# Kernel optimization log

Hardware: AMD Instinct MI355X
Metric: run time of the kernel (lower is better)

## Reference

```python
import jax, jax.numpy as jnp
import numpy as np

H = 256      # term/query/document hidden size (hardcoded .view(-1, 256) in source)
POS_DIM = 4  # nn.Embedding(15, 4)
V = 50000


def gru_cell(x, h, Wih, Whh, bih, bhh):
    """PyTorch-convention GRU cell. x: [B, Din], h: [B, H]."""
    gi = x @ Wih.T + bih
    gh = h @ Whh.T + bhh
    ir, iz, i_n = jnp.split(gi, 3, axis=-1)
    hr, hz, h_n = jnp.split(gh, 3, axis=-1)
    r = jax.nn.sigmoid(ir + hr)
    z = jax.nn.sigmoid(iz + hz)
    n = jnp.tanh(i_n + r * h_n)
    return (1.0 - z) * n + z * h


def _gru_params(key, in_dim, hid):
    k1, k2, k3, k4 = jax.random.split(key, 4)
    s = 1.0 / np.sqrt(hid)
    u = lambda k, shp: jax.random.uniform(k, shp, jnp.float32, -s, s)
    return u(k1, (3 * hid, in_dim)), u(k2, (3 * hid, hid)), u(k3, (3 * hid,)), u(k4, (3 * hid,))


def setup_inputs() -> dict:
    key = jax.random.key(0)
    ks = jax.random.split(key, 16)
    Q, Lq, P, N, Ld = 64, 20, 12, 12, 50
    inp = {}
    inp["query_tokens"] = jax.random.randint(ks[0], (Q, Lq), 0, V, dtype=jnp.int32)
    inp["pos_tokens"] = jax.random.randint(ks[1], (P, Ld), 0, V, dtype=jnp.int32)
    inp["neg_tokens"] = jax.random.randint(ks[2], (N, Ld), 0, V, dtype=jnp.int32)
    # TermEncoder: embedding + GRU cell
    inp["term_emb"] = jax.random.normal(ks[3], (V, H), jnp.float32) * 0.1
    inp["term_Wih"], inp["term_Whh"], inp["term_bih"], inp["term_bhh"] = _gru_params(ks[4], H, H)
    # ContextEncoder: embedding + two GRU cells (content c, attention a)
    inp["doc_emb"] = jax.random.normal(ks[5], (V, H), jnp.float32) * 0.1
    inp["doc_c_Wih"], inp["doc_c_Whh"], inp["doc_c_bih"], inp["doc_c_bhh"] = _gru_params(ks[6], H, H)
    inp["doc_a_Wih"], inp["doc_a_Whh"], inp["doc_a_bih"], inp["doc_a_bhh"] = _gru_params(ks[7], H, H)
    # position embedding (15, 4) + position_dense Linear(H+4 -> H)
    inp["pos_table"] = jax.random.normal(ks[8], (15, POS_DIM), jnp.float32) * 0.1
    sd = 1.0 / np.sqrt(H + POS_DIM)
    inp["posd_W"] = jax.random.uniform(ks[9], (H, H + POS_DIM), jnp.float32, -sd, sd)
    inp["posd_b"] = jax.random.uniform(ks[10], (H,), jnp.float32, -sd, sd)
    # QueryEncoder GRU cell (single step on the memory-augmented query state)
    inp["qry_Wih"], inp["qry_Whh"], inp["qry_bih"], inp["qry_bhh"] = _gru_params(ks[11], H, H)
    return inp


def reference(query_tokens, pos_tokens, neg_tokens,
              term_emb, term_Wih, term_Whh, term_bih, term_bhh,
              doc_emb, doc_c_Wih, doc_c_Whh, doc_c_bih, doc_c_bhh,
              doc_a_Wih, doc_a_Whh, doc_a_bih, doc_a_bhh,
              pos_table, posd_W, posd_b,
              qry_Wih, qry_Whh, qry_bih, qry_bhh):
    f32 = term_emb.dtype

    # --- TermEncoder: run GRU over each query's tokens (batched over Q queries) ---
    q_xs = term_emb[query_tokens]                       # [Q, Lq, H]
    h0q = jnp.zeros((query_tokens.shape[0], H), f32)
    def term_step(h, x):
        return gru_cell(x, h, term_Wih, term_Whh, term_bih, term_bhh), None
    enc_hidden, _ = jax.lax.scan(term_step, h0q, jnp.swapaxes(q_xs, 0, 1))  # [Q, H]

    # --- ContextEncoder: two parallel GRUs over each doc's tokens (batched over docs) ---
    def encode_docs(tokens):
        xs = doc_emb[tokens]                            # [D, Ld, H]
        h0 = jnp.zeros((tokens.shape[0], H), f32)
        def step(carry, x):
            hc, ha = carry
            hc = gru_cell(x, hc, doc_c_Wih, doc_c_Whh, doc_c_bih, doc_c_bhh)
            ha = gru_cell(x, ha, doc_a_Wih, doc_a_Whh, doc_a_bih, doc_a_bhh)
            return (hc, ha), None
        (hc, ha), _ = jax.lax.scan(step, (h0, h0), jnp.swapaxes(xs, 0, 1))
        # position encoding (pos_enc == 1): concat per-doc-index embedding, dense back to H
        pe = pos_table[jnp.arange(tokens.shape[0])]      # [D, 4]
        hc = jnp.concatenate([hc, pe], axis=-1) @ posd_W.T + posd_b
        return hc, ha                                    # [D, H], [D, H]

    pos_c, pos_a = encode_docs(pos_tokens)
    neg_c, neg_a = encode_docs(neg_tokens)

    # --- memory read: softmax(dot(a_vecs, q)) weighted sum of c_vecs, per query ---
    def attend(c, a_vecs, q):
        scores = q @ a_vecs.T                            # [Q, D]
        w = jax.nn.softmax(scores, axis=-1)
        return w @ c                                     # [Q, H]

    q_pos_neg = enc_hidden + attend(pos_c, pos_a, enc_hidden) + attend(neg_c, neg_a, enc_hidden)

    # --- QueryEncoder: one GRU step on the memory-augmented state ---
    h0 = jnp.zeros_like(q_pos_neg)
    q_out = gru_cell(q_pos_neg, h0, qry_Wih, qry_Whh, qry_bih, qry_bhh)  # [Q, H]
    return q_out
```

## Files before the change

kernel.cpp:

```cpp
#include <hip/hip_runtime.h>
#include <hip/hip_fp16.h>
#include <math.h>

#define H 256

typedef _Float16 h2_t __attribute__((ext_vector_type(2)));
union U16x8 { uint4 u; h2_t h[4]; };

#define WS_WTQ   0u
#define WS_PT    196608u
#define WS_WTPT  263168u
#define WS_WTPC  361472u
#define WS_WTPA  459776u
#define WS_GI_T  558080u
#define WS_GI_C  1541120u
#define WS_GI_A  2462720u
#define WS_ENC   3384320u
#define WS_HC    3400704u
#define WS_HA    3406848u
#define WS_HCP   3412992u

__device__ __forceinline__ float sigmoidf_(float x){ return 1.f/(1.f+expf(-x)); }

__global__ __launch_bounds__(256) void k_prep(
    const float* __restrict__ tWhh, const float* __restrict__ cWhh, const float* __restrict__ aWhh,
    const float* __restrict__ qWih, const float* __restrict__ pdW,
    __half* __restrict__ WTPt, __half* __restrict__ WTPc, __half* __restrict__ WTPa,
    float* __restrict__ WTq, float* __restrict__ PT)
{
    const int b = blockIdx.x, tid = threadIdx.x;
    if (b < 2304) {
        const float* in; __half* out; int j;
        if (b < 768)       { in = tWhh; out = WTPt; j = b; }
        else if (b < 1536) { in = cWhh; out = WTPc; j = b - 768; }
        else               { in = aWhh; out = WTPa; j = b - 1536; }
        float v = in[(size_t)j * 256 + tid];
        out[(size_t)(tid >> 3) * 6144 + j * 8 + (tid & 7)] = (__half)v;
        return;
    }
    __shared__ float t[64][65];
    const float* in; float* out; int R, C, bx, by;
    if (b < 2352) { int bb = b - 2304; in = qWih; out = WTq; R = 768; C = 256; bx = bb & 3; by = bb >> 2; }
    else          { int bb = b - 2352; in = pdW;  out = PT;  R = 256; C = 260; bx = bb % 5; by = bb / 5; }
    const int c0 = bx * 64, r0 = by * 64;
    const int cc = tid & 63;
    const int rr = tid >> 6;
#pragma unroll
    for (int s = 0; s < 16; s++) {
        int row = s * 4 + rr;
        if (r0 + row < R && c0 + cc < C)
            t[row][cc] = in[(size_t)(r0 + row) * C + (c0 + cc)];
    }
    __syncthreads();
#pragma unroll
    for (int s = 0; s < 16; s++) {
        int col = s * 4 + rr;
        if (c0 + col < C && r0 + cc < R)
            out[(size_t)(c0 + col) * R + (r0 + cc)] = t[cc][col];
    }
}

__global__ __launch_bounds__(256) void k_gi_gemm(
    const int* __restrict__ qtok, const int* __restrict__ ptok, const int* __restrict__ ntok,
    const float* __restrict__ temb, const float* __restrict__ demb,
    const float* __restrict__ tWih, const float* __restrict__ cWih, const float* __restrict__ aWih,
    const float* __restrict__ tbih, const float* __restrict__ cbih, const float* __restrict__ abih,
    float* __restrict__ gi_term, float* __restrict__ gi_c, float* __restrict__ gi_a)
{
    __shared__ __align__(16) float As[64][68];
    __shared__ __align__(16) float Bs[64][68];
    __shared__ int tok[64];
    __shared__ int vld[64];

    const int bid = blockIdx.x, tid = threadIdx.x;
    const float *Wih, *bih, *emb; float* out; int nrows, seg, mt, nt;
    if (bid < 240)      { seg = 0; int b = bid;       mt = b / 12; nt = b % 12; Wih = tWih; bih = tbih; emb = temb; out = gi_term; nrows = 1280; }
    else if (bid < 468) { seg = 1; int b = bid - 240; mt = b / 12; nt = b % 12; Wih = cWih; bih = cbih; emb = demb; out = gi_c;    nrows = 1200; }
    else                { seg = 2; int b = bid - 468; mt = b / 12; nt = b % 12; Wih = aWih; bih = abih; emb = demb; out = gi_a;    nrows = 1200; }

    if (tid < 64) {
        int rg = mt * 64 + tid;
        int v = rg < nrows;
        int token = 0;
        if (v) {
            if (seg == 0) { int t = rg >> 6, q = rg & 63; token = qtok[q * 20 + t]; }
            else          { int t = rg / 24, d = rg % 24; token = (d < 12) ? ptok[d * 50 + t] : ntok[(d - 12) * 50 + t]; }
        }
        tok[tid] = token; vld[tid] = v;
    }
    __syncthreads();

    float acc[4][4];
#pragma unroll
    for (int i = 0; i < 4; i++)
#pragma unroll
        for (int jj = 0; jj < 4; jj++) acc[i][jj] = 0.f;

    const int r0 = (tid >> 4) << 2;
    const int j0 = (tid & 15) << 2;
    const int jb = nt * 64;
    const int lr = tid & 15;
    const int lk = (tid >> 4) << 2;

    for (int k0 = 0; k0 < 256; k0 += 64) {
#pragma unroll
        for (int s = 0; s < 4; s++) {
            int r = lr + s * 16;
            float4 v4 = *(const float4*)(emb + (size_t)tok[r] * H + k0 + lk);
            As[lk + 0][r] = v4.x; As[lk + 1][r] = v4.y; As[lk + 2][r] = v4.z; As[lk + 3][r] = v4.w;
            float4 w4 = *(const float4*)(Wih + (size_t)(jb + r) * H + k0 + lk);
            Bs[lk + 0][r] = w4.x; Bs[lk + 1][r] = w4.y; Bs[lk + 2][r] = w4.z; Bs[lk + 3][r] = w4.w;
        }
        __syncthreads();
#pragma unroll 8
        for (int k = 0; k < 64; k++) {
            float4 av = *(const float4*)&As[k][r0];
            float4 bv = *(const float4*)&Bs[k][j0];
            acc[0][0] += av.x * bv.x; acc[0][1] += av.x * bv.y; acc[0][2] += av.x * bv.z; acc[0][3] += av.x * bv.w;
            acc[1][0] += av.y * bv.x; acc[1][1] += av.y * bv.y; acc[1][2] += av.y * bv.z; acc[1][3] += av.y * bv.w;
            acc[2][0] += av.z * bv.x; acc[2][1] += av.z * bv.y; acc[2][2] += av.z * bv.z; acc[2][3] += av.z * bv.w;
            acc[3][0] += av.w * bv.x; acc[3][1] += av.w * bv.y; acc[3][2] += av.w * bv.z; acc[3][3] += av.w * bv.w;
        }
        __syncthreads();
    }

    float4 bias = *(const float4*)(bih + jb + j0);
#pragma unroll
    for (int i = 0; i < 4; i++) {
        int r = r0 + i;
        if (!vld[r]) continue;
        int rg = mt * 64 + r;
        float4 o;
        o.x = acc[i][0] + bias.x; o.y = acc[i][1] + bias.y;
        o.z = acc[i][2] + bias.z; o.w = acc[i][3] + bias.w;
        *(float4*)(out + (size_t)rg * 768 + jb + j0) = o;
    }
}

__global__ __launch_bounds__(768, 3) void k_recur4(
    const __half* __restrict__ WTPt, const __half* __restrict__ WTPc, const __half* __restrict__ WTPa,
    const float* __restrict__ tbhh, const float* __restrict__ cbhh, const float* __restrict__ abhh,
    const float* __restrict__ gi_t, const float* __restrict__ gi_c, const float* __restrict__ gi_a,
    float* __restrict__ enc, float* __restrict__ hc, float* __restrict__ ha)
{
    __shared__ __align__(16) __half hhl[H];
    __shared__ __align__(16) float  gh[768];
    const int b = blockIdx.x, tid = threadIdx.x;
    const __half* WTP; const float *bhh, *gi; float* outp; int T, nch, chain;
    if (b < 64)      { WTP = WTPt; bhh = tbhh; gi = gi_t; T = 20; nch = 64; chain = b;      outp = enc; }
    else if (b < 88) { WTP = WTPc; bhh = cbhh; gi = gi_c; T = 50; nch = 24; chain = b - 64; outp = hc; }
    else             { WTP = WTPa; bhh = abhh; gi = gi_a; T = 50; nch = 24; chain = b - 88; outp = ha; }

    const float bj = bhh[tid];

    const uint4* __restrict__ W4 = (const uint4*)WTP;
    uint4 w[32];
#pragma unroll
    for (int k8 = 0; k8 < 32; k8++) w[k8] = W4[k8 * 768 + tid];

    float h = 0.f;
    if (tid < H) hhl[tid] = (__half)0.f;
    __syncthreads();

    const uint4* hh4 = (const uint4*)hhl;
    const float* __restrict__ grow0 = gi + (size_t)chain * 768;
    const size_t gstride = (size_t)nch * 768;

    for (int t = 0; t < T; t++) {
        float a0 = 0.f, a1 = 0.f, a2 = 0.f, a3 = 0.f;
#pragma unroll
        for (int k8 = 0; k8 < 32; k8++) {
            U16x8 hv; hv.u = hh4[k8];
            U16x8 wv; wv.u = w[k8];
            a0 = __builtin_amdgcn_fdot2(wv.h[0], hv.h[0], a0, false);
            a1 = __builtin_amdgcn_fdot2(wv.h[1], hv.h[1], a1, false);
            a2 = __builtin_amdgcn_fdot2(wv.h[2], hv.h[2], a2, false);
            a3 = __builtin_amdgcn_fdot2(wv.h[3], hv.h[3], a3, false);
        }
        gh[tid] = bj + ((a0 + a1) + (a2 + a3));
        __syncthreads();

        if (tid < H) {
            const float* grow = grow0 + (size_t)t * gstride;
            float r = sigmoidf_(grow[tid]       + gh[tid]);
            float z = sigmoidf_(grow[tid + 256] + gh[tid + 256]);
            float n = tanhf(grow[tid + 512] + r * gh[tid + 512]);
            h = (1.f - z) * n + z * h;
            hhl[tid] = (__half)h;
        }
        __syncthreads();
    }
    if (tid < H) outp[(size_t)chain * H + tid] = h;
}

__global__ __launch_bounds__(256) void k_posd(
    const float* __restrict__ PT, const float* __restrict__ pdb,
    const float* __restrict__ ptab, const float* __restrict__ hc_raw,
    float* __restrict__ hcp)
{
    __shared__ __align__(16) float hl[260];
    const int d = blockIdx.x, j = threadIdx.x;
    if (j < 256) hl[j] = hc_raw[d * H + j];
    if (j < 4)   hl[256 + j] = ptab[(d % 12) * 4 + j];
    __syncthreads();
    float acc = pdb[j];
#pragma unroll 4
    for (int k = 0; k < 260; k++) acc += PT[(size_t)k * 256 + j] * hl[k];
    hcp[d * H + j] = acc;
}

__global__ __launch_bounds__(256) void k_final(
    const float* __restrict__ enc, const float* __restrict__ ha, const float* __restrict__ hcp,
    const float* __restrict__ WT_q, const float* __restrict__ qbih, const float* __restrict__ qbhh,
    float* __restrict__ out)
{
    __shared__ __align__(16) float ql[H];
    __shared__ float wts[24];
    __shared__ __align__(16) float qs_l[H];
    const int q = blockIdx.x, j = threadIdx.x;
    ql[j] = enc[q * H + j];
    __syncthreads();
    if (j < 192) {
        int dd = j >> 3, l8 = j & 7;
        float s = 0.f;
        for (int k = l8 * 32; k < l8 * 32 + 32; k++) s += ha[dd * H + k] * ql[k];
        s += __shfl_xor(s, 1); s += __shfl_xor(s, 2); s += __shfl_xor(s, 4);
        if (l8 == 0) wts[dd] = s;
    }
    __syncthreads();
    if (j < 2) {
        int base = j * 12;
        float m = wts[base];
        for (int d = 1; d < 12; d++) m = fmaxf(m, wts[base + d]);
        float sum = 0.f;
        for (int d = 0; d < 12; d++) { float e = expf(wts[base + d] - m); wts[base + d] = e; sum += e; }
        float inv = 1.f / sum;
        for (int d = 0; d < 12; d++) wts[base + d] *= inv;
    }
    __syncthreads();
    float qs = ql[j];
#pragma unroll 4
    for (int d = 0; d < 24; d++) qs += wts[d] * hcp[d * H + j];
    qs_l[j] = qs;
    __syncthreads();
    float ar = qbih[j], az = qbih[j + 256], an = qbih[j + 512];
    const float* wp = WT_q + j;
#pragma unroll 4
    for (int k = 0; k < H; k++) {
        float hv = qs_l[k];
        const float* wk = wp + (size_t)k * 768;
        ar += wk[0] * hv; az += wk[256] * hv; an += wk[512] * hv;
    }
    float r = sigmoidf_(ar + qbhh[j]);
    float z = sigmoidf_(az + qbhh[j + 256]);
    float n = tanhf(an + r * qbhh[j + 512]);
    out[q * H + j] = (1.f - z) * n;
}

extern "C" void kernel_launch(void* const* d_in, const int* in_sizes, int n_in,
                              void* d_out, int out_size, void* d_ws, size_t ws_size,
                              hipStream_t stream)
{
    const int*   qtok = (const int*)d_in[0];
    const int*   ptok = (const int*)d_in[1];
    const int*   ntok = (const int*)d_in[2];
    const float* temb = (const float*)d_in[3];
    const float* tWih = (const float*)d_in[4];
    const float* tWhh = (const float*)d_in[5];
    const float* tbih = (const float*)d_in[6];
    const float* tbhh = (const float*)d_in[7];
    const float* demb = (const float*)d_in[8];
    const float* cWih = (const float*)d_in[9];
    const float* cWhh = (const float*)d_in[10];
    const float* cbih = (const float*)d_in[11];
    const float* cbhh = (const float*)d_in[12];
    const float* aWih = (const float*)d_in[13];
    const float* aWhh = (const float*)d_in[14];
    const float* abih = (const float*)d_in[15];
    const float* abhh = (const float*)d_in[16];
    const float* ptab = (const float*)d_in[17];
    const float* pdW  = (const float*)d_in[18];
    const float* pdb  = (const float*)d_in[19];
    const float* qWih = (const float*)d_in[20];
    const float* qbih = (const float*)d_in[22];
    const float* qbhh = (const float*)d_in[23];

    float* ws  = (float*)d_ws;
    float*  WTq  = ws + WS_WTQ;
    float*  PT   = ws + WS_PT;
    __half* WTPt = (__half*)(ws + WS_WTPT);
    __half* WTPc = (__half*)(ws + WS_WTPC);
    __half* WTPa = (__half*)(ws + WS_WTPA);
    float* GIt = ws + WS_GI_T;
    float* GIc = ws + WS_GI_C;
    float* GIa = ws + WS_GI_A;
    float* ENC = ws + WS_ENC;
    float* HC  = ws + WS_HC;
    float* HA  = ws + WS_HA;
    float* HCP = ws + WS_HCP;

    k_prep<<<2372, 256, 0, stream>>>(tWhh, cWhh, aWhh, qWih, pdW,
                                     WTPt, WTPc, WTPa, WTq, PT);

    k_gi_gemm<<<696, 256, 0, stream>>>(qtok, ptok, ntok, temb, demb,
                                       tWih, cWih, aWih, tbih, cbih, abih,
                                       GIt, GIc, GIa);

    k_recur4<<<112, 768, 0, stream>>>(WTPt, WTPc, WTPa, tbhh, cbhh, abhh,
                                      GIt, GIc, GIa, ENC, HC, HA);

    k_posd<<<24, 256, 0, stream>>>(PT, pdb, ptab, HC, HCP);

    k_final<<<64, 256, 0, stream>>>(ENC, HA, HCP, WTq, qbih, qbhh, (float*)d_out);
}
```

Before: 309.1 us.

## Use MFMA for input GEMM and recurrence, fold position dense into final kernel

The input-gate GEMM now runs on fp16 MFMA instructions, with embeddings converted to half in shared memory. The recurrent GRU matvec uses MFMA 16x16x32 with the hidden vector in one column and the weights pre-swizzled into fragment layout. The position-dense kernel is removed by moving the attention weighting ahead of the dense layer (linearity) inside the final kernel, and the query GRU weights switch to fp16 dot2. Together these aim to replace scalar FP32/dot2 compute with matrix cores and drop one launch, at the cost of lower precision in the input GEMM and wasted MFMA lanes in the matvec.

```diff
diff --git a/kernel.cpp b/kernel.cpp
--- a/kernel.cpp
+++ b/kernel.cpp
@@ -4,222 +4,211 @@
 
 #define H 256
 
-typedef _Float16 h2_t __attribute__((ext_vector_type(2)));
+typedef _Float16 f16x8 __attribute__((ext_vector_type(8)));
+typedef _Float16 f16x4 __attribute__((ext_vector_type(4)));
+typedef float    f32x4 __attribute__((ext_vector_type(4)));
+typedef _Float16 h2_t  __attribute__((ext_vector_type(2)));
 union U16x8 { uint4 u; h2_t h[4]; };
 
-#define WS_WTQ   0u
-#define WS_PT    196608u
-#define WS_WTPT  263168u
-#define WS_WTPC  361472u
-#define WS_WTPA  459776u
-#define WS_GI_T  558080u
-#define WS_GI_C  1541120u
-#define WS_GI_A  2462720u
-#define WS_ENC   3384320u
-#define WS_HC    3400704u
-#define WS_HA    3406848u
-#define WS_HCP   3412992u
+#define WS_WF_T  0u
+#define WS_WF_C  98304u
+#define WS_WF_A  196608u
+#define WS_W16T  294912u
+#define WS_W16C  393216u
+#define WS_W16A  491520u
+#define WS_W16Q  589824u
+#define WS_PT    688128u
+#define WS_GI_T  754688u
+#define WS_GI_C  1737728u
+#define WS_GI_A  2659328u
+#define WS_ENC   3580928u
+#define WS_HC    3597312u
+#define WS_HA    3603456u
 
 __device__ __forceinline__ float sigmoidf_(float x){ return 1.f/(1.f+expf(-x)); }
 
-__global__ __launch_bounds__(256) void k_prep(
+__global__ __launch_bounds__(256) void k_prep2(
     const float* __restrict__ tWhh, const float* __restrict__ cWhh, const float* __restrict__ aWhh,
+    const float* __restrict__ tWih, const float* __restrict__ cWih, const float* __restrict__ aWih,
     const float* __restrict__ qWih, const float* __restrict__ pdW,
-    __half* __restrict__ WTPt, __half* __restrict__ WTPc, __half* __restrict__ WTPa,
-    float* __restrict__ WTq, float* __restrict__ PT)
+    _Float16* __restrict__ WFt, _Float16* __restrict__ WFc, _Float16* __restrict__ WFa,
+    _Float16* __restrict__ W16t, _Float16* __restrict__ W16c, _Float16* __restrict__ W16a,
+    _Float16* __restrict__ W16q, float* __restrict__ PT)
 {
     const int b = blockIdx.x, tid = threadIdx.x;
     if (b < 2304) {
-        const float* in; __half* out; int j;
-        if (b < 768)       { in = tWhh; out = WTPt; j = b; }
-        else if (b < 1536) { in = cWhh; out = WTPc; j = b - 768; }
-        else               { in = aWhh; out = WTPa; j = b - 1536; }
-        float v = in[(size_t)j * 256 + tid];
-        out[(size_t)(tid >> 3) * 6144 + j * 8 + (tid & 7)] = (__half)v;
+        int i = b * 256 + tid;
+        int m = i / 196608, r = i % 196608;
+        const float* in = (m == 0) ? tWhh : (m == 1) ? cWhh : aWhh;
+        _Float16*   out = (m == 0) ? WFt  : (m == 1) ? WFc  : WFa;
+        int f = r >> 9, lane = (r >> 3) & 63, e = r & 7;
+        int row = (f >> 3) * 16 + (lane & 15);
+        int k   = (f & 7) * 32 + ((lane >> 4) & 3) * 8 + e;
+        out[r] = (_Float16)in[row * 256 + k];
         return;
     }
-    __shared__ float t[64][65];
-    const float* in; float* out; int R, C, bx, by;
-    if (b < 2352) { int bb = b - 2304; in = qWih; out = WTq; R = 768; C = 256; bx = bb & 3; by = bb >> 2; }
-    else          { int bb = b - 2352; in = pdW;  out = PT;  R = 256; C = 260; bx = bb % 5; by = bb / 5; }
-    const int c0 = bx * 64, r0 = by * 64;
-    const int cc = tid & 63;
-    const int rr = tid >> 6;
-#pragma unroll
-    for (int s = 0; s < 16; s++) {
-        int row = s * 4 + rr;
-        if (r0 + row < R && c0 + cc < C)
-            t[row][cc] = in[(size_t)(r0 + row) * C + (c0 + cc)];
-    }
-    __syncthreads();
-#pragma unroll
-    for (int s = 0; s < 16; s++) {
-        int col = s * 4 + rr;
-        if (c0 + col < C && r0 + cc < R)
-            out[(size_t)(c0 + col) * R + (r0 + cc)] = t[cc][col];
-    }
-}
-
-__global__ __launch_bounds__(256) void k_gi_gemm(
+    if (b < 5376) {
+        int i = (b - 2304) * 256 + tid;
+        int m = i / 196608, r = i % 196608;
+        const float* in = (m == 0) ? tWih : (m == 1) ? cWih : (m == 2) ? aWih : qWih;
+        _Float16*   out = (m == 0) ? W16t : (m == 1) ? W16c : (m == 2) ? W16a : W16q;
+        out[r] = (_Float16)in[r];
+        return;
+    }
+    {
+        int i = (b - 5376) * 256 + tid;
+        int k = i >> 8, j = i & 255;
+        PT[k * 256 + j] = pdW[j * 260 + k];
+    }
+}
+
+__global__ __launch_bounds__(256) void k_gi2(
     const int* __restrict__ qtok, const int* __restrict__ ptok, const int* __restrict__ ntok,
     const float* __restrict__ temb, const float* __restrict__ demb,
-    const float* __restrict__ tWih, const float* __restrict__ cWih, const float* __restrict__ aWih,
+    const _Float16* __restrict__ W16t, const _Float16* __restrict__ W16c, const _Float16* __restrict__ W16a,
     const float* __restrict__ tbih, const float* __restrict__ cbih, const float* __restrict__ abih,
-    float* __restrict__ gi_term, float* __restrict__ gi_c, float* __restrict__ gi_a)
-{
-    __shared__ __align__(16) float As[64][68];
-    __shared__ __align__(16) float Bs[64][68];
+    float* __restrict__ git, float* __restrict__ gic, float* __restrict__ gia)
+{
+    __shared__ __align__(16) _Float16 At[64 * 264];
     __shared__ int tok[64];
-    __shared__ int vld[64];
 
     const int bid = blockIdx.x, tid = threadIdx.x;
-    const float *Wih, *bih, *emb; float* out; int nrows, seg, mt, nt;
-    if (bid < 240)      { seg = 0; int b = bid;       mt = b / 12; nt = b % 12; Wih = tWih; bih = tbih; emb = temb; out = gi_term; nrows = 1280; }
-    else if (bid < 468) { seg = 1; int b = bid - 240; mt = b / 12; nt = b % 12; Wih = cWih; bih = cbih; emb = demb; out = gi_c;    nrows = 1200; }
-    else                { seg = 2; int b = bid - 468; mt = b / 12; nt = b % 12; Wih = aWih; bih = abih; emb = demb; out = gi_a;    nrows = 1200; }
+    const float *emb, *bih; const _Float16* W16; float* out; int nrows, seg, mt, nt;
+    if (bid < 240)      { seg = 0; int b = bid;       mt = b / 12; nt = b % 12; emb = temb; W16 = W16t; bih = tbih; out = git; nrows = 1280; }
+    else if (bid < 468) { seg = 1; int b = bid - 240; mt = b / 12; nt = b % 12; emb = demb; W16 = W16c; bih = cbih; out = gic; nrows = 1200; }
+    else                { seg = 2; int b = bid - 468; mt = b / 12; nt = b % 12; emb = demb; W16 = W16a; bih = abih; out = gia; nrows = 1200; }
+    const int rowbase = mt * 64, jb = nt * 64;
 
     if (tid < 64) {
-        int rg = mt * 64 + tid;
-        int v = rg < nrows;
+        int rg = rowbase + tid;
         int token = 0;
-        if (v) {
-            if (seg == 0) { int t = rg >> 6, q = rg & 63; token = qtok[q * 20 + t]; }
+        if (rg < nrows) {
+            if (seg == 0) { int t = mt, q = tid; token = qtok[q * 20 + t]; }
             else          { int t = rg / 24, d = rg % 24; token = (d < 12) ? ptok[d * 50 + t] : ntok[(d - 12) * 50 + t]; }
         }
-        tok[tid] = token; vld[tid] = v;
-    }
-    __syncthreads();
-
-    float acc[4][4];
-#pragma unroll
-    for (int i = 0; i < 4; i++)
-#pragma unroll
-        for (int jj = 0; jj < 4; jj++) acc[i][jj] = 0.f;
-
-    const int r0 = (tid >> 4) << 2;
-    const int j0 = (tid & 15) << 2;
-    const int jb = nt * 64;
-    const int lr = tid & 15;
-    const int lk = (tid >> 4) << 2;
-
-    for (int k0 = 0; k0 < 256; k0 += 64) {
-#pragma unroll
-        for (int s = 0; s < 4; s++) {
-            int r = lr + s * 16;
-            float4 v4 = *(const float4*)(emb + (size_t)tok[r] * H + k0 + lk);
-            As[lk + 0][r] = v4.x; As[lk + 1][r] = v4.y; As[lk + 2][r] = v4.z; As[lk + 3][r] = v4.w;
-            float4 w4 = *(const float4*)(Wih + (size_t)(jb + r) * H + k0 + lk);
-            Bs[lk + 0][r] = w4.x; Bs[lk + 1][r] = w4.y; Bs[lk + 2][r] = w4.z; Bs[lk + 3][r] = w4.w;
-        }
-        __syncthreads();
-#pragma unroll 8
-        for (int k = 0; k < 64; k++) {
-            float4 av = *(const float4*)&As[k][r0];
-            float4 bv = *(const float4*)&Bs[k][j0];
-            acc[0][0] += av.x * bv.x; acc[0][1] += av.x * bv.y; acc[0][2] += av.x * bv.z; acc[0][3] += av.x * bv.w;
-            acc[1][0] += av.y * bv.x; acc[1][1] += av.y * bv.y; acc[1][2] += av.y * bv.z; acc[1][3] += av.y * bv.w;
-            acc[2][0] += av.z * bv.x; acc[2][1] += av.z * bv.y; acc[2][2] += av.z * bv.z; acc[2][3] += av.z * bv.w;
-            acc[3][0] += av.w * bv.x; acc[3][1] += av.w * bv.y; acc[3][2] += av.w * bv.z; acc[3][3] += av.w * bv.w;
-        }
-        __syncthreads();
-    }
-
-    float4 bias = *(const float4*)(bih + jb + j0);
-#pragma unroll
-    for (int i = 0; i < 4; i++) {
-        int r = r0 + i;
-        if (!vld[r]) continue;
-        int rg = mt * 64 + r;
-        float4 o;
-        o.x = acc[i][0] + bias.x; o.y = acc[i][1] + bias.y;
-        o.z = acc[i][2] + bias.z; o.w = acc[i][3] + bias.w;
-        *(float4*)(out + (size_t)rg * 768 + jb + j0) = o;
-    }
-}
-
-__global__ __launch_bounds__(768, 3) void k_recur4(
-    const __half* __restrict__ WTPt, const __half* __restrict__ WTPc, const __half* __restrict__ WTPa,
+        tok[tid] = token;
+    }
+    __syncthreads();
+
+#pragma unroll
+    for (int i = 0; i < 16; i++) {
+        int idx = i * 256 + tid;
+        int r = idx >> 6, c4 = idx & 63;
+        float4 v = *(const float4*)(emb + (size_t)tok[r] * H + c4 * 4);
+        f16x4 hv = { (_Float16)v.x, (_Float16)v.y, (_Float16)v.z, (_Float16)v.w };
+        *(f16x4*)(At + r * 264 + c4 * 4) = hv;
+    }
+    __syncthreads();
+
+    const int wave = tid >> 6, lane = tid & 63;
+    const int rt = wave;
+    const int kg = (lane >> 4) & 3;
+
+    f16x8 af[8];
+    const _Float16* abase = At + (rt * 16 + (lane & 15)) * 264 + kg * 8;
+#pragma unroll
+    for (int kt = 0; kt < 8; kt++) af[kt] = *(const f16x8*)(abase + kt * 32);
+
+#pragma unroll
+    for (int ct = 0; ct < 4; ct++) {
+        const int col = jb + ct * 16 + (lane & 15);
+        const _Float16* wrow = W16 + (size_t)col * H + kg * 8;
+        f32x4 acc = {0.f, 0.f, 0.f, 0.f};
+#pragma unroll
+        for (int kt = 0; kt < 8; kt++) {
+            f16x8 bf = *(const f16x8*)(wrow + kt * 32);
+            acc = __builtin_amdgcn_mfma_f32_16x16x32_f16(af[kt], bf, acc, 0, 0, 0);
+        }
+        float bias = bih[col];
+#pragma unroll
+        for (int e = 0; e < 4; e++) {
+            int row_g = rowbase + rt * 16 + kg * 4 + e;
+            if (row_g < nrows)
+                out[(size_t)row_g * 768 + col] = acc[e] + bias;
+        }
+    }
+}
+
+__global__ __launch_bounds__(768) void k_recur5(
+    const _Float16* __restrict__ WFt, const _Float16* __restrict__ WFc, const _Float16* __restrict__ WFa,
     const float* __restrict__ tbhh, const float* __restrict__ cbhh, const float* __restrict__ abhh,
     const float* __restrict__ gi_t, const float* __restrict__ gi_c, const float* __restrict__ gi_a,
     float* __restrict__ enc, float* __restrict__ hc, float* __restrict__ ha)
 {
-    __shared__ __align__(16) __half hhl[H];
-    __shared__ __align__(16) float  gh[768];
+    __shared__ __align__(16) _Float16 hhl[H];
+    __shared__ __align__(16) float    ghl[768];
+
     const int b = blockIdx.x, tid = threadIdx.x;
-    const __half* WTP; const float *bhh, *gi; float* outp; int T, nch, chain;
-    if (b < 64)      { WTP = WTPt; bhh = tbhh; gi = gi_t; T = 20; nch = 64; chain = b;      outp = enc; }
-    else if (b < 88) { WTP = WTPc; bhh = cbhh; gi = gi_c; T = 50; nch = 24; chain = b - 64; outp = hc; }
-    else             { WTP = WTPa; bhh = abhh; gi = gi_a; T = 50; nch = 24; chain = b - 88; outp = ha; }
-
-    const float bj = bhh[tid];
-
-    const uint4* __restrict__ W4 = (const uint4*)WTP;
-    uint4 w[32];
-#pragma unroll
-    for (int k8 = 0; k8 < 32; k8++) w[k8] = W4[k8 * 768 + tid];
-
-    float h = 0.f;
-    if (tid < H) hhl[tid] = (__half)0.f;
-    __syncthreads();
-
-    const uint4* hh4 = (const uint4*)hhl;
-    const float* __restrict__ grow0 = gi + (size_t)chain * 768;
-    const size_t gstride = (size_t)nch * 768;
+    const _Float16* WF; const float *bhh, *gi; float* outp; int T, nch, chain;
+    if (b < 64)      { WF = WFt; bhh = tbhh; gi = gi_t; T = 20; nch = 64; chain = b;      outp = enc; }
+    else if (b < 88) { WF = WFc; bhh = cbhh; gi = gi_c; T = 50; nch = 24; chain = b - 64; outp = hc; }
+    else             { WF = WFa; bhh = abhh; gi = gi_a; T = 50; nch = 24; chain = b - 88; outp = ha; }
+
+    const int wave = tid >> 6, lane = tid & 63;
+    const int grp = (lane >> 4) & 3;
+    const bool extr = (lane & 15) == 0;
+
+    const f16x8* __restrict__ WFp = (const f16x8*)WF;
+    f16x8 wf[32];
+#pragma unroll
+    for (int i = 0; i < 32; i++) wf[i] = WFp[(size_t)(wave * 32 + i) * 64 + lane];
+    asm volatile("" ::: "memory");
+
+    float h = 0.f, br = 0.f, bz = 0.f, bn = 0.f;
+    if (tid < H) {
+        br = bhh[tid]; bz = bhh[tid + 256]; bn = bhh[tid + 512];
+        hhl[tid] = (_Float16)0.f;
+    }
+    __syncthreads();
 
     for (int t = 0; t < T; t++) {
-        float a0 = 0.f, a1 = 0.f, a2 = 0.f, a3 = 0.f;
-#pragma unroll
-        for (int k8 = 0; k8 < 32; k8++) {
-            U16x8 hv; hv.u = hh4[k8];
-            U16x8 wv; wv.u = w[k8];
-            a0 = __builtin_amdgcn_fdot2(wv.h[0], hv.h[0], a0, false);
-            a1 = __builtin_amdgcn_fdot2(wv.h[1], hv.h[1], a1, false);
-            a2 = __builtin_amdgcn_fdot2(wv.h[2], hv.h[2], a2, false);
-            a3 = __builtin_amdgcn_fdot2(wv.h[3], hv.h[3], a3, false);
-        }
-        gh[tid] = bj + ((a0 + a1) + (a2 + a3));
+        f32x4 acc0 = {0.f,0.f,0.f,0.f}, acc1 = {0.f,0.f,0.f,0.f};
+        f32x4 acc2 = {0.f,0.f,0.f,0.f}, acc3 = {0.f,0.f,0.f,0.f};
+#pragma unroll
+        for (int kt = 0; kt < 8; kt++) {
+            f16x8 bv = {0,0,0,0,0,0,0,0};
+            if (extr) bv = *(const f16x8*)(hhl + kt * 32 + grp * 8);
+            acc0 = __builtin_amdgcn_mfma_f32_16x16x32_f16(wf[0 * 8 + kt], bv, acc0, 0, 0, 0);
+            acc1 = __builtin_amdgcn_mfma_f32_16x16x32_f16(wf[1 * 8 + kt], bv, acc1, 0, 0, 0);
+            acc2 = __builtin_amdgcn_mfma_f32_16x16x32_f16(wf[2 * 8 + kt], bv, acc2, 0, 0, 0);
+            acc3 = __builtin_amdgcn_mfma_f32_16x16x32_f16(wf[3 * 8 + kt], bv, acc3, 0, 0, 0);
+        }
+        if (extr) {
+            *(f32x4*)(ghl + wave * 64 +  0 + grp * 4) = acc0;
+            *(f32x4*)(ghl + wave * 64 + 16 + grp * 4) = acc1;
+            *(f32x4*)(ghl + wave * 64 + 32 + grp * 4) = acc2;
+            *(f32x4*)(ghl + wave * 64 + 48 + grp * 4) = acc3;
+        }
         __syncthreads();
-
         if (tid < H) {
-            const float* grow = grow0 + (size_t)t * gstride;
-            float r = sigmoidf_(grow[tid]       + gh[tid]);
-            float z = sigmoidf_(grow[tid + 256] + gh[tid + 256]);
-            float n = tanhf(grow[tid + 512] + r * gh[tid + 512]);
+            const float* __restrict__ grow = gi + (size_t)(t * nch + chain) * 768;
+            float r = sigmoidf_(grow[tid]       + br + ghl[tid]);
+            float z = sigmoidf_(grow[tid + 256] + bz + ghl[tid + 256]);
+            float n = tanhf(grow[tid + 512] + r * (bn + ghl[tid + 512]));
             h = (1.f - z) * n + z * h;
-            hhl[tid] = (__half)h;
+            hhl[tid] = (_Float16)h;
         }
         __syncthreads();
     }
     if (tid < H) outp[(size_t)chain * H + tid] = h;
 }
 
-__global__ __launch_bounds__(256) void k_posd(
-    const float* __restrict__ PT, const float* __restrict__ pdb,
-    const float* __restrict__ ptab, const float* __restrict__ hc_raw,
-    float* __restrict__ hcp)
-{
-    __shared__ __align__(16) float hl[260];
-    const int d = blockIdx.x, j = threadIdx.x;
-    if (j < 256) hl[j] = hc_raw[d * H + j];
-    if (j < 4)   hl[256 + j] = ptab[(d % 12) * 4 + j];
-    __syncthreads();
-    float acc = pdb[j];
-#pragma unroll 4
-    for (int k = 0; k < 260; k++) acc += PT[(size_t)k * 256 + j] * hl[k];
-    hcp[d * H + j] = acc;
-}
-
-__global__ __launch_bounds__(256) void k_final(
-    const float* __restrict__ enc, const float* __restrict__ ha, const float* __restrict__ hcp,
-    const float* __restrict__ WT_q, const float* __restrict__ qbih, const float* __restrict__ qbhh,
+__global__ __launch_bounds__(256) void k_final2(
+    const float* __restrict__ enc, const float* __restrict__ ha, const float* __restrict__ hc,
+    const float* __restrict__ ptab, const float* __restrict__ PT, const float* __restrict__ pdb,
+    const _Float16* __restrict__ qW16, const float* __restrict__ qbih, const float* __restrict__ qbhh,
     float* __restrict__ out)
 {
     __shared__ __align__(16) float ql[H];
+    __shared__ __align__(16) float csl[H];
+    __shared__ float csp[4];
     __shared__ float wts[24];
-    __shared__ __align__(16) float qs_l[H];
+    __shared__ __align__(16) _Float16 q2h[H];
+
     const int q = blockIdx.x, j = threadIdx.x;
     ql[j] = enc[q * H + j];
     __syncthreads();
+
     if (j < 192) {
         int dd = j >> 3, l8 = j & 7;
         float s = 0.f;
@@ -238,22 +227,51 @@
         for (int d = 0; d < 12; d++) wts[base + d] *= inv;
     }
     __syncthreads();
-    float qs = ql[j];
+
+    {
+        float cs = 0.f;
 #pragma unroll 4
-    for (int d = 0; d < 24; d++) qs += wts[d] * hcp[d * H + j];
-    qs_l[j] = qs;
-    __syncthreads();
-    float ar = qbih[j], az = qbih[j + 256], an = qbih[j + 512];
-    const float* wp = WT_q + j;
+        for (int d = 0; d < 24; d++) cs += wts[d] * hc[d * H + j];
+        csl[j] = cs;
+    }
+    if (j < 4) {
+        float cp = 0.f;
+        for (int d = 0; d < 24; d++) cp += wts[d] * ptab[(d % 12) * 4 + j];
+        csp[j] = cp;
+    }
+    __syncthreads();
+
+    float att = 2.f * pdb[j];
 #pragma unroll 4
-    for (int k = 0; k < H; k++) {
-        float hv = qs_l[k];
-        const float* wk = wp + (size_t)k * 768;
-        ar += wk[0] * hv; az += wk[256] * hv; an += wk[512] * hv;
-    }
-    float r = sigmoidf_(ar + qbhh[j]);
-    float z = sigmoidf_(az + qbhh[j + 256]);
-    float n = tanhf(an + r * qbhh[j + 512]);
+    for (int k = 0; k < 256; k++) att += csl[k] * PT[(size_t)k * 256 + j];
+#pragma unroll
+    for (int k = 0; k < 4; k++)   att += csp[k] * PT[(size_t)(256 + k) * 256 + j];
+
+    float q2 = ql[j] + att;
+    q2h[j] = (_Float16)q2;
+    __syncthreads();
+
+    const uint4* q4 = (const uint4*)q2h;
+    const uint4* w0 = (const uint4*)(qW16 + (size_t)(j      ) * H);
+    const uint4* w1 = (const uint4*)(qW16 + (size_t)(j + 256) * H);
+    const uint4* w2 = (const uint4*)(qW16 + (size_t)(j + 512) * H);
+    float ar = 0.f, az = 0.f, an = 0.f;
+#pragma unroll 8
+    for (int k8 = 0; k8 < 32; k8++) {
+        U16x8 hv; hv.u = q4[k8];
+        U16x8 a; a.u = w0[k8];
+        U16x8 bb; bb.u = w1[k8];
+        U16x8 c; c.u = w2[k8];
+#pragma unroll
+        for (int p = 0; p < 4; p++) {
+            ar = __builtin_amdgcn_fdot2(a.h[p],  hv.h[p], ar, false);
+            az = __builtin_amdgcn_fdot2(bb.h[p], hv.h[p], az, false);
+            an = __builtin_amdgcn_fdot2(c.h[p],  hv.h[p], an, false);
+        }
+    }
+    float r = sigmoidf_(ar + qbih[j]       + qbhh[j]);
+    float z = sigmoidf_(az + qbih[j + 256] + qbhh[j + 256]);
+    float n = tanhf(an + qbih[j + 512] + r * qbhh[j + 512]);
     out[q * H + j] = (1.f - z) * n;
 }
 
@@ -285,31 +303,32 @@
     const float* qbih = (const float*)d_in[22];
     const float* qbhh = (const float*)d_in[23];
 
-    float* ws  = (float*)d_ws;
-    float*  WTq  = ws + WS_WTQ;
-    float*  PT   = ws + WS_PT;
-    __half* WTPt = (__half*)(ws + WS_WTPT);
-    __half* WTPc = (__half*)(ws + WS_WTPC);
-    __half* WTPa = (__half*)(ws + WS_WTPA);
+    float* ws = (float*)d_ws;
+    _Float16* WFt  = (_Float16*)(ws + WS_WF_T);
+    _Float16* WFc  = (_Float16*)(ws + WS_WF_C);
+    _Float16* WFa  = (_Float16*)(ws + WS_WF_A);
+    _Float16* W16t = (_Float16*)(ws + WS_W16T);
+    _Float16* W16c = (_Float16*)(ws + WS_W16C);
+    _Float16* W16a = (_Float16*)(ws + WS_W16A);
+    _Float16* W16q = (_Float16*)(ws + WS_W16Q);
+    float* PT  = ws + WS_PT;
     float* GIt = ws + WS_GI_T;
     float* GIc = ws + WS_GI_C;
     float* GIa = ws + WS_GI_A;
     float* ENC = ws + WS_ENC;
     float* HC  = ws + WS_HC;
     float* HA  = ws + WS_HA;
-    float* HCP = ws + WS_HCP;
-
-    k_prep<<<2372, 256, 0, stream>>>(tWhh, cWhh, aWhh, qWih, pdW,
-                                     WTPt, WTPc, WTPa, WTq, PT);
-
-    k_gi_gemm<<<696, 256, 0, stream>>>(qtok, ptok, ntok, temb, demb,
-                                       tWih, cWih, aWih, tbih, cbih, abih,
-                                       GIt, GIc, GIa);
-
-    k_recur4<<<112, 768, 0, stream>>>(WTPt, WTPc, WTPa, tbhh, cbhh, abhh,
+
+    k_prep2<<<5636, 256, 0, stream>>>(tWhh, cWhh, aWhh, tWih, cWih, aWih, qWih, pdW,
+                                      WFt, WFc, WFa, W16t, W16c, W16a, W16q, PT);
+
+    k_gi2<<<696, 256, 0, stream>>>(qtok, ptok, ntok, temb, demb,
+                                   W16t, W16c, W16a, tbih, cbih, abih,
+                                   GIt, GIc, GIa);
+
+    k_recur5<<<112, 768, 0, stream>>>(WFt, WFc, WFa, tbhh, cbhh, abhh,
                                       GIt, GIc, GIa, ENC, HC, HA);
 
-    k_posd<<<24, 256, 0, stream>>>(PT, pdb, ptab, HC, HCP);
-
-    k_final<<<64, 256, 0, stream>>>(ENC, HA, HCP, WTq, qbih, qbhh, (float*)d_out);
-}
+    k_final2<<<64, 256, 0, stream>>>(ENC, HA, HC, ptab, PT, pdb,
+                                     W16q, qbih, qbhh, (float*)d_out);
+}
```

After: 293.5 us. 1.05x faster.
